# Kernel optimization log

Measured on AMD Instinct MI355X. Metric: run time of the kernel, lower is better.

## Reference

```python
import jax, jax.numpy as jnp
import numpy as np

DIM = 1024
NUM_HEADS = 16
HEAD_DIM = DIM // NUM_HEADS  # 64
GRID = 32                    # ft_seq_len = pt_seq_len = 32 -> seq_len = 1024
ROPE_DIM = HEAD_DIM // 2     # 32; repeat_interleave(2)+concat -> 64 = head_dim
EPS = 1e-6


def _rope_tables():
    theta = 10000.0
    freqs = 1.0 / theta ** (np.arange(0, ROPE_DIM, 2, dtype=np.float32) / ROPE_DIM)  # [16]
    positions = np.arange(GRID, dtype=np.float32) / GRID * GRID                      # [32]
    f = np.einsum('n,d->nd', positions, freqs)                                       # [32,16]
    f = np.repeat(f, 2, axis=-1)                                                     # [32,32]
    f2 = np.concatenate([np.broadcast_to(f[:, None, :], (GRID, GRID, ROPE_DIM)),
                         np.broadcast_to(f[None, :, :], (GRID, GRID, ROPE_DIM))],
                        axis=-1).reshape(GRID * GRID, 2 * ROPE_DIM)                  # [1024,64]
    return np.cos(f2).astype(np.float32), np.sin(f2).astype(np.float32)


def setup_inputs() -> dict:
    key = jax.random.key(0)
    ks = jax.random.split(key, 8)
    B, S = 8, GRID * GRID
    cos_np, sin_np = _rope_tables()
    s = 0.02
    return {
        'hidden_states': jax.random.normal(ks[0], (B, S, DIM), jnp.float32),
        'W_qkv': jax.random.normal(ks[1], (DIM, 3 * DIM), jnp.float32) * s,
        'b_qkv': jnp.zeros((3 * DIM,), jnp.float32),
        'qn_w': jnp.ones((HEAD_DIM,), jnp.float32),
        'qn_b': jnp.zeros((HEAD_DIM,), jnp.float32),
        'kn_w': jnp.ones((HEAD_DIM,), jnp.float32),
        'kn_b': jnp.zeros((HEAD_DIM,), jnp.float32),
        'W_proj': jax.random.normal(ks[2], (DIM, DIM), jnp.float32) * s,
        'b_proj': jnp.zeros((DIM,), jnp.float32),
        'freqs_cos': jnp.asarray(cos_np),
        'freqs_sin': jnp.asarray(sin_np),
    }


def _rotate_half(x):
    x2 = x.reshape(*x.shape[:-1], -1, 2)
    a, b = x2[..., 0], x2[..., 1]
    return jnp.stack((-b, a), axis=-1).reshape(x.shape)


def _layernorm(x, w, b):
    mu = jnp.mean(x, axis=-1, keepdims=True)
    var = jnp.mean(jnp.square(x - mu), axis=-1, keepdims=True)
    return (x - mu) * jax.lax.rsqrt(var + EPS) * w + b


def reference(hidden_states, W_qkv, b_qkv, qn_w, qn_b, kn_w, kn_b, W_proj, b_proj, freqs_cos, freqs_sin):
    B, S, C = hidden_states.shape
    qkv = hidden_states @ W_qkv + b_qkv                               # [B,S,3C]
    qkv = qkv.reshape(B, S, 3, NUM_HEADS, HEAD_DIM).transpose(2, 0, 3, 1, 4)
    q, k, v = qkv[0], qkv[1], qkv[2]                                  # [B,H,S,D]
    q = _layernorm(q, qn_w, qn_b)
    k = _layernorm(k, kn_w, kn_b)
    # RoPE: cos/sin broadcast over batch and heads; tables are [S, D]
    q = q * freqs_cos + _rotate_half(q) * freqs_sin
    k = k * freqs_cos + _rotate_half(k) * freqs_sin
    scale = 1.0 / jnp.sqrt(jnp.asarray(HEAD_DIM, q.dtype))
    scores = jnp.einsum('bhqd,bhkd->bhqk', q, k) * scale
    attn = jax.nn.softmax(scores, axis=-1)
    out = jnp.einsum('bhqk,bhkd->bhqd', attn, v)                      # [B,H,S,D]
    out = out.transpose(0, 2, 1, 3).reshape(B, S, C)
    return out @ W_proj + b_proj
```

## Files before the change

### kernel.cpp

```cpp
#include <hip/hip_runtime.h>
#include <hip/hip_bf16.h>

#define DEV __device__ __forceinline__

typedef __attribute__((ext_vector_type(8))) short bf16x8;
typedef __attribute__((ext_vector_type(4))) short short4v;
typedef __attribute__((ext_vector_type(4))) float f32x4;
typedef __attribute__((ext_vector_type(4))) int int4v;

static constexpr int BATCH = 8;
static constexpr int SEQ   = 1024;
static constexpr int CDIM  = 1024;
static constexpr int NH    = 16;
static constexpr int HD    = 64;
static constexpr int N3    = 3072;

DEV short f2bf(float x) {
    __hip_bfloat16 h = __float2bfloat16(x);
    return __builtin_bit_cast(short, h);
}
DEV float bf2f(short x) {
    unsigned u = ((unsigned)(unsigned short)x) << 16;
    return __builtin_bit_cast(float, u);
}
DEV float exp2_hw(float x) {
    float r;
    asm("v_exp_f32 %0, %1" : "=v"(r) : "v"(x));
    return r;
}

typedef __attribute__((address_space(1))) const unsigned gas_u32;
typedef __attribute__((address_space(3))) unsigned las_u32;
DEV void gll16(const void* g, void* l) {
    __builtin_amdgcn_global_load_lds((gas_u32*)g, (las_u32*)l, 16, 0, 0);
}

__global__ __launch_bounds__(256) void k_prep(
    const float* __restrict__ hidden, short* __restrict__ hbf,
    const float* __restrict__ Wq, short* __restrict__ WqT,
    const float* __restrict__ Wp, short* __restrict__ WpT) {
    __shared__ float tile[32][33];
    int bid = blockIdx.x, tid = threadIdx.x;
    if (bid < 4096) {
        int i = (bid * 256 + tid) * 8;
        float4 a = *(const float4*)(hidden + i);
        float4 b = *(const float4*)(hidden + i + 4);
        bf16x8 o;
        o[0] = f2bf(a.x); o[1] = f2bf(a.y); o[2] = f2bf(a.z); o[3] = f2bf(a.w);
        o[4] = f2bf(b.x); o[5] = f2bf(b.y); o[6] = f2bf(b.z); o[7] = f2bf(b.w);
        *(bf16x8*)(hbf + i) = o;
        return;
    }
    const float* src; short* dst; int K, N, bx, by;
    if (bid < 4096 + 3072) {
        int bt = bid - 4096; src = Wq; dst = WqT; K = CDIM; N = N3;
        bx = bt % (N3 / 32); by = bt / (N3 / 32);
    } else {
        int bt = bid - 7168; src = Wp; dst = WpT; K = CDIM; N = CDIM;
        bx = bt % (CDIM / 32); by = bt / (CDIM / 32);
    }
    int tx = tid & 31, ty = tid >> 5;
    int n0 = bx * 32, k0 = by * 32;
    for (int i = 0; i < 32; i += 8)
        tile[ty + i][tx] = src[(size_t)(k0 + ty + i) * N + n0 + tx];
    __syncthreads();
    for (int i = 0; i < 32; i += 8)
        dst[(size_t)(n0 + ty + i) * K + k0 + tx] = f2bf(tile[tx][ty + i]);
}

__global__ __launch_bounds__(512, 2) void k_gemm256(
    const short* __restrict__ A, const short* __restrict__ Bt,
    const float* __restrict__ bias, short* __restrict__ Cout,
    int M, int N, int K) {
    __shared__ char lds[2][2][2][16384];
    const int tid = threadIdx.x;
    const int wid = tid >> 6, l = tid & 63;
    const int lr = l & 15, lk = l >> 4;
    const int wm = wid >> 2, wn = wid & 3;
    const int nbn = N >> 8;
    const int nwg = gridDim.x;
    const int q8 = nwg >> 3;
    const int wg = (blockIdx.x & 7) * q8 + (blockIdx.x >> 3);
    const int m0 = (wg / nbn) << 8, n0 = (wg % nbn) << 8;
    const int NT = K >> 6;

    auto stA = [&](int buf, int h, int kt) {
#pragma unroll
        for (int j = 0; j < 2; ++j) {
            int L = (wid * 64 + l + j * 512) * 16;
            int b = L ^ (((L >> 7) & 7) << 4);
            int hr = b >> 7, ke = (b & 127) >> 1;
            int grow = m0 + (hr & 63) + h * 64 + ((hr >> 6) << 7);
            gll16(A + (size_t)grow * K + kt * 64 + ke,
                  &lds[buf][0][h][wid * 1024 + j * 8192]);
        }
    };
    auto stB = [&](int buf, int h, int kt) {
#pragma unroll
        for (int j = 0; j < 2; ++j) {
            int L = (wid * 64 + l + j * 512) * 16;
            int b = L ^ (((L >> 7) & 7) << 4);
            int hr = b >> 7, ke = (b & 127) >> 1;
            int grow = n0 + ((hr >> 5) << 6) + h * 32 + (hr & 31);
            gll16(Bt + (size_t)grow * K + kt * 64 + ke,
                  &lds[buf][1][h][wid * 1024 + j * 8192]);
        }
    };
    auto rdA = [&](int buf, int h, int mi, int ks) -> bf16x8 {
        int b = (wm * 64 + mi * 16 + lr) * 128 + ks * 64 + lk * 16;
        return *(const bf16x8*)&lds[buf][0][h][b ^ (((b >> 7) & 7) << 4)];
    };
    auto rdB = [&](int buf, int h, int ni, int ks) -> bf16x8 {
        int b = (wn * 32 + ni * 16 + lr) * 128 + ks * 64 + lk * 16;
        return *(const bf16x8*)&lds[buf][1][h][b ^ (((b >> 7) & 7) << 4)];
    };

    f32x4 acc[8][4] = {};
    stA(0, 0, 0); stB(0, 0, 0); stB(0, 1, 0); stA(0, 1, 0);
    stA(1, 0, 1); stB(1, 0, 1); stB(1, 1, 1);
    asm volatile("s_waitcnt vmcnt(6)" ::: "memory");
    __builtin_amdgcn_s_barrier();

    bf16x8 aF[4][2], b0[2][2], b1[2][2];
#pragma unroll
    for (int ni = 0; ni < 2; ++ni) { b0[ni][0] = rdB(0, 0, ni, 0); b0[ni][1] = rdB(0, 0, ni, 1); }

    for (int T = 0; T < NT; ++T) {
        const int p = T & 1;
#pragma unroll
        for (int mi = 0; mi < 4; ++mi) { aF[mi][0] = rdA(p, 0, mi, 0); aF[mi][1] = rdA(p, 0, mi, 1); }
        if (T + 1 < NT) stA(p ^ 1, 1, T + 1);
        __builtin_amdgcn_s_barrier();
        asm volatile("s_waitcnt lgkmcnt(0)" ::: "memory");
        __builtin_amdgcn_s_setprio(1);
#pragma unroll
        for (int mi = 0; mi < 4; ++mi)
#pragma unroll
            for (int ni = 0; ni < 2; ++ni)
#pragma unroll
                for (int ks = 0; ks < 2; ++ks)
                    acc[mi][ni] = __builtin_amdgcn_mfma_f32_16x16x32_bf16(aF[mi][ks], b0[ni][ks], acc[mi][ni], 0, 0, 0);
        __builtin_amdgcn_s_setprio(0);
        __builtin_amdgcn_s_barrier();
#pragma unroll
        for (int ni = 0; ni < 2; ++ni) { b1[ni][0] = rdB(p, 1, ni, 0); b1[ni][1] = rdB(p, 1, ni, 1); }
        if (T + 2 < NT) stA(p, 0, T + 2);
        __builtin_amdgcn_s_barrier();
        asm volatile("s_waitcnt lgkmcnt(0)" ::: "memory");
        __builtin_amdgcn_s_setprio(1);
#pragma unroll
        for (int mi = 0; mi < 4; ++mi)
#pragma unroll
            for (int ni = 0; ni < 2; ++ni)
#pragma unroll
                for (int ks = 0; ks < 2; ++ks)
                    acc[mi][2 + ni] = __builtin_amdgcn_mfma_f32_16x16x32_bf16(aF[mi][ks], b1[ni][ks], acc[mi][2 + ni], 0, 0, 0);
        __builtin_amdgcn_s_setprio(0);
        __builtin_amdgcn_s_barrier();
#pragma unroll
        for (int mi = 0; mi < 4; ++mi) { aF[mi][0] = rdA(p, 1, mi, 0); aF[mi][1] = rdA(p, 1, mi, 1); }
        if (T + 2 < NT) stB(p, 0, T + 2);
        __builtin_amdgcn_s_barrier();
        asm volatile("s_waitcnt lgkmcnt(0)" ::: "memory");
        __builtin_amdgcn_s_setprio(1);
#pragma unroll
        for (int mi = 0; mi < 4; ++mi)
#pragma unroll
            for (int ni = 0; ni < 2; ++ni)
#pragma unroll
                for (int ks = 0; ks < 2; ++ks)
                    acc[4 + mi][2 + ni] = __builtin_amdgcn_mfma_f32_16x16x32_bf16(aF[mi][ks], b1[ni][ks], acc[4 + mi][2 + ni], 0, 0, 0);
        __builtin_amdgcn_s_setprio(0);
        __builtin_amdgcn_s_barrier();
        if (T + 2 < NT) {
            stB(p, 1, T + 2);
            asm volatile("s_waitcnt vmcnt(6)" ::: "memory");
        } else if (T + 1 < NT) {
            asm volatile("s_waitcnt vmcnt(0)" ::: "memory");
        }
        __builtin_amdgcn_s_barrier();
        __builtin_amdgcn_s_setprio(1);
#pragma unroll
        for (int mi = 0; mi < 4; ++mi)
#pragma unroll
            for (int ni = 0; ni < 2; ++ni)
#pragma unroll
                for (int ks = 0; ks < 2; ++ks)
                    acc[4 + mi][ni] = __builtin_amdgcn_mfma_f32_16x16x32_bf16(aF[mi][ks], b0[ni][ks], acc[4 + mi][ni], 0, 0, 0);
        __builtin_amdgcn_s_setprio(0);
        if (T + 1 < NT) {
#pragma unroll
            for (int ni = 0; ni < 2; ++ni) { b0[ni][0] = rdB(p ^ 1, 0, ni, 0); b0[ni][1] = rdB(p ^ 1, 0, ni, 1); }
        }
        __builtin_amdgcn_s_barrier();
    }
#pragma unroll
    for (int ami = 0; ami < 8; ++ami) {
        int grow = m0 + wm * 128 + (ami >> 2) * 64 + (ami & 3) * 16 + lk * 4;
#pragma unroll
        for (int ani = 0; ani < 4; ++ani) {
            int gcol = n0 + wn * 64 + (ani >> 1) * 32 + (ani & 1) * 16 + lr;
            float bv = bias[gcol];
#pragma unroll
            for (int r = 0; r < 4; ++r)
                Cout[(size_t)(grow + r) * N + gcol] = f2bf(acc[ami][ani][r] + bv);
        }
    }
}

template <bool OUT_BF16>
__global__ __launch_bounds__(256) void k_gemm(
    const short* __restrict__ A, const short* __restrict__ Bt,
    const float* __restrict__ bias, void* __restrict__ Cout,
    int M, int N, int K) {
    constexpr int BM = 128, BN = 128, BK = 32;
    __shared__ short As[BM * BK];
    __shared__ short Bs[BN * BK];
    int tid = threadIdx.x;
    int nbn = N / BN;
    int bm = blockIdx.x / nbn, bn = blockIdx.x % nbn;
    int m0 = bm * BM, n0 = bn * BN;
    int w = tid >> 6, l = tid & 63;
    int wm = (w >> 1) * 64, wn = (w & 1) * 64;
    int lr = l & 15, lk = l >> 4;
    f32x4 acc[4][4] = {};
    int rowS = w * 32 + (l >> 2);
    int colS = (l & 3) * 8;
    for (int k0 = 0; k0 < K; k0 += BK) {
        const short* ga = A  + (size_t)(m0 + rowS) * K + k0 + colS;
        const short* gb = Bt + (size_t)(n0 + rowS) * K + k0 + colS;
        gll16(ga,          &As[(w * 32) * BK]);
        gll16(ga + 16 * K, &As[(w * 32 + 16) * BK]);
        gll16(gb,          &Bs[(w * 32) * BK]);
        gll16(gb + 16 * K, &Bs[(w * 32 + 16) * BK]);
        __syncthreads();
        bf16x8 af[4], bfr[4];
#pragma unroll
        for (int mi = 0; mi < 4; ++mi) af[mi]  = *(const bf16x8*)&As[(wm + mi * 16 + lr) * BK + lk * 8];
#pragma unroll
        for (int ni = 0; ni < 4; ++ni) bfr[ni] = *(const bf16x8*)&Bs[(wn + ni * 16 + lr) * BK + lk * 8];
#pragma unroll
        for (int mi = 0; mi < 4; ++mi)
#pragma unroll
            for (int ni = 0; ni < 4; ++ni)
                acc[mi][ni] = __builtin_amdgcn_mfma_f32_16x16x32_bf16(af[mi], bfr[ni], acc[mi][ni], 0, 0, 0);
        __syncthreads();
    }
#pragma unroll
    for (int mi = 0; mi < 4; ++mi)
#pragma unroll
        for (int ni = 0; ni < 4; ++ni) {
            int col = n0 + wn + ni * 16 + lr;
            float bv = bias[col];
#pragma unroll
            for (int r = 0; r < 4; ++r) {
                int row = m0 + wm + mi * 16 + lk * 4 + r;
                float v = acc[mi][ni][r] + bv;
                if (OUT_BF16) ((short*)Cout)[(size_t)row * N + col] = f2bf(v);
                else          ((float*)Cout)[(size_t)row * N + col] = v;
            }
        }
}

__global__ __launch_bounds__(256) void k_lnrope_vt(
    const short* __restrict__ qkv,
    const float* __restrict__ qn_w, const float* __restrict__ qn_b,
    const float* __restrict__ kn_w, const float* __restrict__ kn_b,
    const float* __restrict__ fcos, const float* __restrict__ fsin,
    short* __restrict__ q, short* __restrict__ k, short* __restrict__ vt) {
    __shared__ short tile[64][72];
    int bid = blockIdx.x, tid = threadIdx.x;
    if (bid < 8192) {
        int l = tid & 63;
        int gw = bid * 4 + (tid >> 6);
        int job = gw * 8 + (l >> 3);
        int sub = l & 7;
        int h = job & 15;
        int t = job >> 4;
        int which = t & 1;
        int bs = t >> 1;
        int s = bs & 1023, b = bs >> 10;
        bf16x8 xv = *(const bf16x8*)(qkv + (size_t)bs * N3 + which * CDIM + h * HD + sub * 8);
        float x[8];
#pragma unroll
        for (int j = 0; j < 8; ++j) x[j] = bf2f(xv[j]);
        float sum = 0.f;
#pragma unroll
        for (int j = 0; j < 8; ++j) sum += x[j];
        sum += __shfl_xor(sum, 1); sum += __shfl_xor(sum, 2); sum += __shfl_xor(sum, 4);
        float mu = sum * (1.f / 64.f);
        float var = 0.f;
#pragma unroll
        for (int j = 0; j < 8; ++j) { x[j] -= mu; var += x[j] * x[j]; }
        var += __shfl_xor(var, 1); var += __shfl_xor(var, 2); var += __shfl_xor(var, 4);
        float rs = rsqrtf(var * (1.f / 64.f) + 1e-6f);
        const float* wv = which ? kn_w : qn_w;
        const float* bb = which ? kn_b : qn_b;
        float wl[8], bl[8], cl[8], sl[8];
        *(float4*)&wl[0] = *(const float4*)(wv + sub * 8);
        *(float4*)&wl[4] = *(const float4*)(wv + sub * 8 + 4);
        *(float4*)&bl[0] = *(const float4*)(bb + sub * 8);
        *(float4*)&bl[4] = *(const float4*)(bb + sub * 8 + 4);
        *(float4*)&cl[0] = *(const float4*)(fcos + s * HD + sub * 8);
        *(float4*)&cl[4] = *(const float4*)(fcos + s * HD + sub * 8 + 4);
        *(float4*)&sl[0] = *(const float4*)(fsin + s * HD + sub * 8);
        *(float4*)&sl[4] = *(const float4*)(fsin + s * HD + sub * 8 + 4);
        float y[8];
#pragma unroll
        for (int j = 0; j < 8; ++j) y[j] = x[j] * rs * wl[j] + bl[j];
        bf16x8 ov;
#pragma unroll
        for (int j = 0; j < 8; j += 2) {
            float e = y[j] * cl[j] - y[j + 1] * sl[j];
            float o = y[j + 1] * cl[j + 1] + y[j] * sl[j + 1];
            ov[j] = f2bf(e); ov[j + 1] = f2bf(o);
        }
        short* dst = which ? k : q;
        *(bf16x8*)(dst + ((size_t)(b * NH + h) * SEQ + s) * HD + sub * 8) = ov;
        return;
    }
    int vb = bid - 8192;
    int st = vb & 15, bh = vb >> 4;
    int h = bh & 15, b = bh >> 4;
    int s0 = st * 64;
    const short* src = qkv + (size_t)b * SEQ * N3 + 2 * CDIM + h * HD;
    for (int c = tid; c < 512; c += 256) {
        int sr = c >> 3, cg = c & 7;
        *(int4v*)&tile[sr][cg * 8] = *(const int4v*)&src[(size_t)(s0 + sr) * N3 + cg * 8];
    }
    __syncthreads();
    short* dst = vt + (size_t)bh * HD * SEQ + s0;
    for (int c = tid; c < 512; c += 256) {
        int d = c >> 3, sg = c & 7;
        short tmp[8];
#pragma unroll
        for (int j = 0; j < 8; ++j) tmp[j] = tile[sg * 8 + j][d];
        *(int4v*)&dst[(size_t)d * SEQ + sg * 8] = *(const int4v*)tmp;
    }
}

__global__ __launch_bounds__(512) void k_attn(
    const short* __restrict__ q, const short* __restrict__ k, const short* __restrict__ vt,
    short* __restrict__ out ) {
    constexpr int KVB = 64;
    constexpr int NT = SEQ / KVB;
    __shared__ short Ks[2][KVB * 64];
    __shared__ short Vs[2][64 * KVB];
    int tid = threadIdx.x, w = tid >> 6, l = tid & 63;
    int bid = blockIdx.x;
    int swz = (bid & 7) * 128 + (bid >> 3);
    int bh = swz >> 3;
    int q0 = (swz & 7) * 128;
    const short* qb = q  + (size_t)bh * SEQ * HD;
    const short* kb = k  + (size_t)bh * SEQ * HD;
    const short* vb = vt + (size_t)bh * HD * SEQ;
    int lr = l & 15, lk = l >> 4;
    int qrow = q0 + w * 16 + lr;
    bf16x8 qB[2];
    qB[0] = *(const bf16x8*)&qb[(size_t)qrow * HD + lk * 8];
    qB[1] = *(const bf16x8*)&qb[(size_t)qrow * HD + 32 + lk * 8];
    f32x4 accO[4] = {};
    float ls_acc = 0.f;
    int g0 = 2 * (lk & 1);
    bool hi = (lk >> 1) != 0;
    constexpr float SC2 = 0.125f * 1.44269504f;

    int srow = tid >> 3, scg = tid & 7;
    int soff = srow * 128 + ((scg * 16) ^ ((srow & 7) << 4));
    const short* kg = kb + (size_t)srow * HD + scg * 8;
    const short* vg = vb + (size_t)srow * SEQ + scg * 8;
    int4v kreg = *(const int4v*)kg;
    int4v vreg = *(const int4v*)vg;
    *(int4v*)((char*)Ks[0] + soff) = kreg;
    *(int4v*)((char*)Vs[0] + soff) = vreg;

    for (int t = 0; t < NT; ++t) {
        __syncthreads();
        int cur = t & 1;
        if (t + 1 < NT) {
            kreg = *(const int4v*)(kg + (size_t)(t + 1) * KVB * HD);
            vreg = *(const int4v*)(vg + (t + 1) * KVB);
        }
        f32x4 sc[4];
        __builtin_amdgcn_s_setprio(1);
#pragma unroll
        for (int nf = 0; nf < 4; ++nf) {
            f32x4 a = {};
#pragma unroll
            for (int ks = 0; ks < 2; ++ks) {
                int row = nf * 16 + lr;
                bf16x8 kf = *(const bf16x8*)((const char*)Ks[cur] + row * 128 +
                                             ((ks * 64 + lk * 16) ^ ((row & 7) << 4)));
                a = __builtin_amdgcn_mfma_f32_16x16x32_bf16(kf, qB[ks], a, 0, 0, 0);
            }
            sc[nf] = a;
        }
        __builtin_amdgcn_s_setprio(0);
        float ps[4][4];
#pragma unroll
        for (int nf = 0; nf < 4; ++nf)
#pragma unroll
            for (int r = 0; r < 4; ++r) {
                float p = exp2_hw(sc[nf][r] * SC2);
                ps[nf][r] = p;
                ls_acc += p;
            }
        unsigned pwd[4][2];
#pragma unroll
        for (int nf = 0; nf < 4; ++nf)
#pragma unroll
            for (int jj = 0; jj < 2; ++jj)
                pwd[nf][jj] = (unsigned)(unsigned short)f2bf(ps[nf][2 * jj]) |
                              ((unsigned)(unsigned short)f2bf(ps[nf][2 * jj + 1]) << 16);
#pragma unroll
        for (int c = 0; c < 2; ++c) {
            unsigned wds[4];
#pragma unroll
            for (int w2 = 0; w2 < 4; ++w2) {
                int src = lr + 16 * (g0 + (w2 >> 1));
                unsigned a0 = (unsigned)__shfl((int)pwd[2 * c][w2 & 1], src);
                unsigned a1 = (unsigned)__shfl((int)pwd[2 * c + 1][w2 & 1], src);
                wds[w2] = hi ? a1 : a0;
            }
            int4v wi = { (int)wds[0], (int)wds[1], (int)wds[2], (int)wds[3] };
            bf16x8 pf = __builtin_bit_cast(bf16x8, wi);
            __builtin_amdgcn_s_setprio(1);
#pragma unroll
            for (int df = 0; df < 4; ++df) {
                int row = df * 16 + lr;
                bf16x8 vf = *(const bf16x8*)((const char*)Vs[cur] + row * 128 +
                                             ((c * 64 + lk * 16) ^ ((row & 7) << 4)));
                accO[df] = __builtin_amdgcn_mfma_f32_16x16x32_bf16(vf, pf, accO[df], 0, 0, 0);
            }
            __builtin_amdgcn_s_setprio(0);
        }
        if (t + 1 < NT) {
            *(int4v*)((char*)Ks[cur ^ 1] + soff) = kreg;
            *(int4v*)((char*)Vs[cur ^ 1] + soff) = vreg;
        }
    }
    float lsum = ls_acc;
    lsum += __shfl_xor(lsum, 16);
    lsum += __shfl_xor(lsum, 32);
    float inv = 1.f / lsum;
    int b = bh >> 4, h = bh & 15;
    int qg = q0 + w * 16 + lr;
#pragma unroll
    for (int df = 0; df < 4; ++df) {
        short4v o4;
#pragma unroll
        for (int r = 0; r < 4; ++r) o4[r] = f2bf(accO[df][r] * inv);
        *(short4v*)&out[((size_t)(b * SEQ + qg)) * CDIM + h * HD + df * 16 + lk * 4] = o4;
    }
}

extern "C" void kernel_launch(void* const* d_in, const int* in_sizes, int n_in,
                              void* d_out, int out_size, void* d_ws, size_t ws_size,
                              hipStream_t stream) {
    const float* hidden = (const float*)d_in[0];
    const float* W_qkv  = (const float*)d_in[1];
    const float* b_qkv  = (const float*)d_in[2];
    const float* qn_w   = (const float*)d_in[3];
    const float* qn_b   = (const float*)d_in[4];
    const float* kn_w   = (const float*)d_in[5];
    const float* kn_b   = (const float*)d_in[6];
    const float* W_proj = (const float*)d_in[7];
    const float* b_proj = (const float*)d_in[8];
    const float* fcos   = (const float*)d_in[9];
    const float* fsin   = (const float*)d_in[10];
    float* out = (float*)d_out;

    const size_t SZ_HBF    = (size_t)BATCH * SEQ * CDIM * 2;
    const size_t SZ_WQKVT  = (size_t)N3 * CDIM * 2;
    const size_t SZ_WPROJT = (size_t)CDIM * CDIM * 2;
    const size_t SZ_QKV    = (size_t)BATCH * SEQ * N3 * 2;
    const size_t SZ_HEAD   = (size_t)BATCH * NH * SEQ * HD * 2;

    char* ws = (char*)d_ws;
    short* hbf    = (short*)ws; ws += SZ_HBF;
    short* wqkvT  = (short*)ws; ws += SZ_WQKVT;
    short* wprojT = (short*)ws; ws += SZ_WPROJT;
    short* qkv    = (short*)ws; ws += SZ_QKV;
    short* qh     = (short*)ws; ws += SZ_HEAD;
    short* kh     = (short*)ws; ws += SZ_HEAD;
    short* vt     = (short*)ws; ws += SZ_HEAD;
    short* attn_o = hbf;

    size_t needed = SZ_HBF + SZ_WQKVT + SZ_WPROJT + SZ_QKV + 3 * SZ_HEAD;
    if (ws_size < needed) return;

    k_prep<<<4096 + 3072 + 1024, 256, 0, stream>>>(hidden, hbf, W_qkv, wqkvT, W_proj, wprojT);

    k_gemm256<<<(BATCH * SEQ / 256) * (N3 / 256), 512, 0, stream>>>(
        hbf, wqkvT, b_qkv, qkv, BATCH * SEQ, N3, CDIM);

    k_lnrope_vt<<<8192 + 2048, 256, 0, stream>>>(
        qkv, qn_w, qn_b, kn_w, kn_b, fcos, fsin, qh, kh, vt);

    k_attn<<<BATCH * NH * (SEQ / 128), 512, 0, stream>>>(qh, kh, vt, attn_o);

    k_gemm<false><<<(BATCH * SEQ / 128) * (CDIM / 128), 256, 0, stream>>>(
        attn_o, wprojT, b_proj, out, BATCH * SEQ, CDIM, CDIM);
}
```

Before: 197.0 us.

## Replace both GEMMs with a shared 256x128 pipelined MFMA kernel template

The 256x256 QKV GEMM kernel is reworked into a templated 256x128 tile kernel with a simpler two-phase pipeline: one B tile and two A halves per stage, double-buffered. The same kernel now also handles the output projection, replacing the naive 128x128 single-buffered GEMM. The QKV launch doubles its workgroup count for better CU occupancy and load balance. In exchange each A tile is reused across only half as many output columns, which adds global and LDS traffic.

```diff
diff --git a/kernel.cpp b/kernel.cpp
--- a/kernel.cpp
+++ b/kernel.cpp
@@ -68,20 +68,21 @@
         dst[(size_t)(n0 + ty + i) * K + k0 + tx] = f2bf(tile[tx][ty + i]);
 }
 
-__global__ __launch_bounds__(512, 2) void k_gemm256(
+template <bool OUT_BF16>
+__global__ __launch_bounds__(512, 2) void k_gemmA(
     const short* __restrict__ A, const short* __restrict__ Bt,
-    const float* __restrict__ bias, short* __restrict__ Cout,
+    const float* __restrict__ bias, void* __restrict__ Cout,
     int M, int N, int K) {
-    __shared__ char lds[2][2][2][16384];
+    __shared__ char lds[2][3][16384];
     const int tid = threadIdx.x;
     const int wid = tid >> 6, l = tid & 63;
     const int lr = l & 15, lk = l >> 4;
     const int wm = wid >> 2, wn = wid & 3;
-    const int nbn = N >> 8;
+    const int nbn = N >> 7;
     const int nwg = gridDim.x;
     const int q8 = nwg >> 3;
     const int wg = (blockIdx.x & 7) * q8 + (blockIdx.x >> 3);
-    const int m0 = (wg / nbn) << 8, n0 = (wg % nbn) << 8;
+    const int m0 = (wg / nbn) << 8, n0 = (wg % nbn) << 7;
     const int NT = K >> 6;
 
     auto stA = [&](int buf, int h, int kt) {
@@ -92,41 +93,40 @@
             int hr = b >> 7, ke = (b & 127) >> 1;
             int grow = m0 + (hr & 63) + h * 64 + ((hr >> 6) << 7);
             gll16(A + (size_t)grow * K + kt * 64 + ke,
-                  &lds[buf][0][h][wid * 1024 + j * 8192]);
+                  &lds[buf][h][wid * 1024 + j * 8192]);
         }
     };
-    auto stB = [&](int buf, int h, int kt) {
+    auto stB = [&](int buf, int kt) {
 #pragma unroll
         for (int j = 0; j < 2; ++j) {
             int L = (wid * 64 + l + j * 512) * 16;
             int b = L ^ (((L >> 7) & 7) << 4);
             int hr = b >> 7, ke = (b & 127) >> 1;
-            int grow = n0 + ((hr >> 5) << 6) + h * 32 + (hr & 31);
+            int grow = n0 + hr;
             gll16(Bt + (size_t)grow * K + kt * 64 + ke,
-                  &lds[buf][1][h][wid * 1024 + j * 8192]);
+                  &lds[buf][2][wid * 1024 + j * 8192]);
         }
     };
     auto rdA = [&](int buf, int h, int mi, int ks) -> bf16x8 {
         int b = (wm * 64 + mi * 16 + lr) * 128 + ks * 64 + lk * 16;
-        return *(const bf16x8*)&lds[buf][0][h][b ^ (((b >> 7) & 7) << 4)];
+        return *(const bf16x8*)&lds[buf][h][b ^ (((b >> 7) & 7) << 4)];
     };
-    auto rdB = [&](int buf, int h, int ni, int ks) -> bf16x8 {
+    auto rdB = [&](int buf, int ni, int ks) -> bf16x8 {
         int b = (wn * 32 + ni * 16 + lr) * 128 + ks * 64 + lk * 16;
-        return *(const bf16x8*)&lds[buf][1][h][b ^ (((b >> 7) & 7) << 4)];
+        return *(const bf16x8*)&lds[buf][2][b ^ (((b >> 7) & 7) << 4)];
     };
 
-    f32x4 acc[8][4] = {};
-    stA(0, 0, 0); stB(0, 0, 0); stB(0, 1, 0); stA(0, 1, 0);
-    stA(1, 0, 1); stB(1, 0, 1); stB(1, 1, 1);
-    asm volatile("s_waitcnt vmcnt(6)" ::: "memory");
+    f32x4 acc[8][2] = {};
+    stA(0, 0, 0); stB(0, 0); stA(0, 1, 0);
+    stA(1, 0, 1); stB(1, 1);
+    asm volatile("s_waitcnt vmcnt(4)" ::: "memory");
     __builtin_amdgcn_s_barrier();
 
-    bf16x8 aF[4][2], b0[2][2], b1[2][2];
-#pragma unroll
-    for (int ni = 0; ni < 2; ++ni) { b0[ni][0] = rdB(0, 0, ni, 0); b0[ni][1] = rdB(0, 0, ni, 1); }
-
+    bf16x8 aF[4][2], bB[2][2];
     for (int T = 0; T < NT; ++T) {
         const int p = T & 1;
+#pragma unroll
+        for (int ni = 0; ni < 2; ++ni) { bB[ni][0] = rdB(p, ni, 0); bB[ni][1] = rdB(p, ni, 1); }
 #pragma unroll
         for (int mi = 0; mi < 4; ++mi) { aF[mi][0] = rdA(p, 0, mi, 0); aF[mi][1] = rdA(p, 0, mi, 1); }
         if (T + 1 < NT) stA(p ^ 1, 1, T + 1);
@@ -139,12 +139,17 @@
             for (int ni = 0; ni < 2; ++ni)
 #pragma unroll
                 for (int ks = 0; ks < 2; ++ks)
-                    acc[mi][ni] = __builtin_amdgcn_mfma_f32_16x16x32_bf16(aF[mi][ks], b0[ni][ks], acc[mi][ni], 0, 0, 0);
+                    acc[mi][ni] = __builtin_amdgcn_mfma_f32_16x16x32_bf16(aF[mi][ks], bB[ni][ks], acc[mi][ni], 0, 0, 0);
         __builtin_amdgcn_s_setprio(0);
         __builtin_amdgcn_s_barrier();
 #pragma unroll
-        for (int ni = 0; ni < 2; ++ni) { b1[ni][0] = rdB(p, 1, ni, 0); b1[ni][1] = rdB(p, 1, ni, 1); }
-        if (T + 2 < NT) stA(p, 0, T + 2);
+        for (int mi = 0; mi < 4; ++mi) { aF[mi][0] = rdA(p, 1, mi, 0); aF[mi][1] = rdA(p, 1, mi, 1); }
+        if (T + 2 < NT) {
+            stA(p, 0, T + 2); stB(p, T + 2);
+            asm volatile("s_waitcnt vmcnt(4)" ::: "memory");
+        } else {
+            asm volatile("s_waitcnt vmcnt(0)" ::: "memory");
+        }
         __builtin_amdgcn_s_barrier();
         asm volatile("s_waitcnt lgkmcnt(0)" ::: "memory");
         __builtin_amdgcn_s_setprio(1);
@@ -154,112 +159,25 @@
             for (int ni = 0; ni < 2; ++ni)
 #pragma unroll
                 for (int ks = 0; ks < 2; ++ks)
-                    acc[mi][2 + ni] = __builtin_amdgcn_mfma_f32_16x16x32_bf16(aF[mi][ks], b1[ni][ks], acc[mi][2 + ni], 0, 0, 0);
+                    acc[4 + mi][ni] = __builtin_amdgcn_mfma_f32_16x16x32_bf16(aF[mi][ks], bB[ni][ks], acc[4 + mi][ni], 0, 0, 0);
         __builtin_amdgcn_s_setprio(0);
         __builtin_amdgcn_s_barrier();
-#pragma unroll
-        for (int mi = 0; mi < 4; ++mi) { aF[mi][0] = rdA(p, 1, mi, 0); aF[mi][1] = rdA(p, 1, mi, 1); }
-        if (T + 2 < NT) stB(p, 0, T + 2);
-        __builtin_amdgcn_s_barrier();
-        asm volatile("s_waitcnt lgkmcnt(0)" ::: "memory");
-        __builtin_amdgcn_s_setprio(1);
-#pragma unroll
-        for (int mi = 0; mi < 4; ++mi)
-#pragma unroll
-            for (int ni = 0; ni < 2; ++ni)
-#pragma unroll
-                for (int ks = 0; ks < 2; ++ks)
-                    acc[4 + mi][2 + ni] = __builtin_amdgcn_mfma_f32_16x16x32_bf16(aF[mi][ks], b1[ni][ks], acc[4 + mi][2 + ni], 0, 0, 0);
-        __builtin_amdgcn_s_setprio(0);
-        __builtin_amdgcn_s_barrier();
-        if (T + 2 < NT) {
-            stB(p, 1, T + 2);
-            asm volatile("s_waitcnt vmcnt(6)" ::: "memory");
-        } else if (T + 1 < NT) {
-            asm volatile("s_waitcnt vmcnt(0)" ::: "memory");
-        }
-        __builtin_amdgcn_s_barrier();
-        __builtin_amdgcn_s_setprio(1);
-#pragma unroll
-        for (int mi = 0; mi < 4; ++mi)
-#pragma unroll
-            for (int ni = 0; ni < 2; ++ni)
-#pragma unroll
-                for (int ks = 0; ks < 2; ++ks)
-                    acc[4 + mi][ni] = __builtin_amdgcn_mfma_f32_16x16x32_bf16(aF[mi][ks], b0[ni][ks], acc[4 + mi][ni], 0, 0, 0);
-        __builtin_amdgcn_s_setprio(0);
-        if (T + 1 < NT) {
-#pragma unroll
-            for (int ni = 0; ni < 2; ++ni) { b0[ni][0] = rdB(p ^ 1, 0, ni, 0); b0[ni][1] = rdB(p ^ 1, 0, ni, 1); }
-        }
-        __builtin_amdgcn_s_barrier();
     }
 #pragma unroll
     for (int ami = 0; ami < 8; ++ami) {
         int grow = m0 + wm * 128 + (ami >> 2) * 64 + (ami & 3) * 16 + lk * 4;
 #pragma unroll
-        for (int ani = 0; ani < 4; ++ani) {
-            int gcol = n0 + wn * 64 + (ani >> 1) * 32 + (ani & 1) * 16 + lr;
+        for (int ani = 0; ani < 2; ++ani) {
+            int gcol = n0 + wn * 32 + ani * 16 + lr;
             float bv = bias[gcol];
 #pragma unroll
-            for (int r = 0; r < 4; ++r)
-                Cout[(size_t)(grow + r) * N + gcol] = f2bf(acc[ami][ani][r] + bv);
-        }
-    }
-}
-
-template <bool OUT_BF16>
-__global__ __launch_bounds__(256) void k_gemm(
-    const short* __restrict__ A, const short* __restrict__ Bt,
-    const float* __restrict__ bias, void* __restrict__ Cout,
-    int M, int N, int K) {
-    constexpr int BM = 128, BN = 128, BK = 32;
-    __shared__ short As[BM * BK];
-    __shared__ short Bs[BN * BK];
-    int tid = threadIdx.x;
-    int nbn = N / BN;
-    int bm = blockIdx.x / nbn, bn = blockIdx.x % nbn;
-    int m0 = bm * BM, n0 = bn * BN;
-    int w = tid >> 6, l = tid & 63;
-    int wm = (w >> 1) * 64, wn = (w & 1) * 64;
-    int lr = l & 15, lk = l >> 4;
-    f32x4 acc[4][4] = {};
-    int rowS = w * 32 + (l >> 2);
-    int colS = (l & 3) * 8;
-    for (int k0 = 0; k0 < K; k0 += BK) {
-        const short* ga = A  + (size_t)(m0 + rowS) * K + k0 + colS;
-        const short* gb = Bt + (size_t)(n0 + rowS) * K + k0 + colS;
-        gll16(ga,          &As[(w * 32) * BK]);
-        gll16(ga + 16 * K, &As[(w * 32 + 16) * BK]);
-        gll16(gb,          &Bs[(w * 32) * BK]);
-        gll16(gb + 16 * K, &Bs[(w * 32 + 16) * BK]);
-        __syncthreads();
-        bf16x8 af[4], bfr[4];
-#pragma unroll
-        for (int mi = 0; mi < 4; ++mi) af[mi]  = *(const bf16x8*)&As[(wm + mi * 16 + lr) * BK + lk * 8];
-#pragma unroll
-        for (int ni = 0; ni < 4; ++ni) bfr[ni] = *(const bf16x8*)&Bs[(wn + ni * 16 + lr) * BK + lk * 8];
-#pragma unroll
-        for (int mi = 0; mi < 4; ++mi)
-#pragma unroll
-            for (int ni = 0; ni < 4; ++ni)
-                acc[mi][ni] = __builtin_amdgcn_mfma_f32_16x16x32_bf16(af[mi], bfr[ni], acc[mi][ni], 0, 0, 0);
-        __syncthreads();
-    }
-#pragma unroll
-    for (int mi = 0; mi < 4; ++mi)
-#pragma unroll
-        for (int ni = 0; ni < 4; ++ni) {
-            int col = n0 + wn + ni * 16 + lr;
-            float bv = bias[col];
-#pragma unroll
             for (int r = 0; r < 4; ++r) {
-                int row = m0 + wm + mi * 16 + lk * 4 + r;
-                float v = acc[mi][ni][r] + bv;
-                if (OUT_BF16) ((short*)Cout)[(size_t)row * N + col] = f2bf(v);
-                else          ((float*)Cout)[(size_t)row * N + col] = v;
+                float v = acc[ami][ani][r] + bv;
+                if (OUT_BF16) ((short*)Cout)[(size_t)(grow + r) * N + gcol] = f2bf(v);
+                else          ((float*)Cout)[(size_t)(grow + r) * N + gcol] = v;
             }
         }
+    }
 }
 
 __global__ __launch_bounds__(256) void k_lnrope_vt(
@@ -491,7 +409,7 @@
 
     k_prep<<<4096 + 3072 + 1024, 256, 0, stream>>>(hidden, hbf, W_qkv, wqkvT, W_proj, wprojT);
 
-    k_gemm256<<<(BATCH * SEQ / 256) * (N3 / 256), 512, 0, stream>>>(
+    k_gemmA<true><<<(BATCH * SEQ / 256) * (N3 / 128), 512, 0, stream>>>(
         hbf, wqkvT, b_qkv, qkv, BATCH * SEQ, N3, CDIM);
 
     k_lnrope_vt<<<8192 + 2048, 256, 0, stream>>>(
@@ -499,6 +417,6 @@
 
     k_attn<<<BATCH * NH * (SEQ / 128), 512, 0, stream>>>(qh, kh, vt, attn_o);
 
-    k_gemm<false><<<(BATCH * SEQ / 128) * (CDIM / 128), 256, 0, stream>>>(
+    k_gemmA<false><<<(BATCH * SEQ / 256) * (CDIM / 128), 512, 0, stream>>>(
         attn_o, wprojT, b_proj, out, BATCH * SEQ, CDIM, CDIM);
 }
```

Measured after the change: 188.9 us. 4.1% less time.
